# Kernel tuning notes

Measured on AMD Instinct MI355X. Metric: run time of the kernel, lower is better.

The kernel has to match this reference:

```python
import jax, jax.numpy as jnp
import numpy as np

EPS = 1e-5

def _layernorm(x, g, b):
    mu = jnp.mean(x, axis=-1, keepdims=True)
    var = jnp.mean(jnp.square(x - mu), axis=-1, keepdims=True)
    return (x - mu) * jax.lax.rsqrt(var + EPS) * g + b

def _knn_gather(x, idx):
    # x: (B, M, C), idx: (B, N, K) -> (B, N, K, C)
    return jax.vmap(lambda m, i: m[i])(x, idx)

def setup_inputs() -> dict:
    key = jax.random.key(0)
    B, N, M, K, C = 1, 8192, 8192, 32, 256
    ks = jax.random.split(key, 24)
    w = lambda k, *s: (jax.random.normal(k, s, dtype=jnp.float32) * 0.02)
    inp = {
        "input_states": jax.random.normal(ks[0], (B, N, C), dtype=jnp.float32),
        "memory_states": jax.random.normal(ks[1], (B, M, C), dtype=jnp.float32),
        "indices": jax.random.randint(ks[2], (B, N, K), 0, M, dtype=jnp.int32),
        "input_coord": jax.random.normal(ks[3], (B, N, 3), dtype=jnp.float32),
        "memory_coord": jax.random.normal(ks[4], (B, M, 3), dtype=jnp.float32),
        "attention_mask": jnp.ones((B, N, K), dtype=jnp.float32),
        "Wq": w(ks[5], C, C), "bq": jnp.zeros((C,), jnp.float32),
        "Wk": w(ks[6], C, C), "bk": jnp.zeros((C,), jnp.float32),
        "Wv": w(ks[7], C, C), "bv": jnp.zeros((C,), jnp.float32),
        "Wo": w(ks[8], C, C), "bo": jnp.zeros((C,), jnp.float32),
        "ln1_g": jnp.ones((C,), jnp.float32), "ln1_b": jnp.zeros((C,), jnp.float32),
        "Wrpe": w(ks[9], C // 2, 3), "brpe": jnp.zeros((C // 2,), jnp.float32),
        "We": w(ks[10], 2 * C, C), "be": jnp.zeros((2 * C,), jnp.float32),
        "Ws": w(ks[11], C, 2 * C), "bs": jnp.zeros((C,), jnp.float32),
        "ln2_g": jnp.ones((C,), jnp.float32), "ln2_b": jnp.zeros((C,), jnp.float32),
    }
    return inp

def reference(input_states, memory_states, indices, input_coord, memory_coord,
              attention_mask, Wq, bq, Wk, bk, Wv, bv, Wo, bo, ln1_g, ln1_b,
              Wrpe, brpe, We, be, Ws, bs, ln2_g, ln2_b):
    B, N, C = input_states.shape
    H = 8
    Ch = C // H
    q = input_states @ Wq.T + bq                                   # (B,N,C)
    k = _knn_gather(memory_states @ Wk.T + bk, indices)            # (B,N,K,C)
    v = _knn_gather(memory_states @ Wv.T + bv, indices)            # (B,N,K,C)
    # rotary positional encoding on relative coordinates
    rel = _knn_gather(memory_coord, indices) - input_coord[:, :, None, :]  # (B,N,K,3)
    ang = rel @ Wrpe.T + brpe                                      # (B,N,K,C/2)
    cos, sin = jnp.cos(ang), jnp.sin(ang)
    k2 = k.reshape(*k.shape[:-1], C // 2, 2)
    x0, x1 = k2[..., 0], k2[..., 1]
    k = jnp.stack([x0 * cos - x1 * sin, x0 * sin + x1 * cos], axis=-1).reshape(k.shape)
    # multi-head attention over K gathered neighbors
    qh = q.reshape(B, N, H, Ch)
    kh = k.reshape(B, N, -1, H, Ch)
    vh = v.reshape(B, N, -1, H, Ch)
    scores = jnp.einsum('bnhc,bnkhc->bhnk', qh, kh) / np.sqrt(Ch).astype(np.float32)
    scores = scores - 1e6 * (1.0 - attention_mask[:, None, :, :])
    attn = jax.nn.softmax(scores, axis=-1)
    hidden = jnp.einsum('bhnk,bnkhc->bnhc', attn, vh).reshape(B, N, C)
    hidden = hidden @ Wo.T + bo
    out = _layernorm(hidden + input_states, ln1_g, ln1_b)
    ff = jax.nn.relu(out @ We.T + be) @ Ws.T + bs
    return _layernorm(out + ff, ln2_g, ln2_b)
```

## Files before the change

kernel.cpp:

```cpp
#include <hip/hip_runtime.h>
#include <hip/hip_bf16.h>
#include <stdint.h>

typedef __attribute__((ext_vector_type(8))) __bf16 bf16x8;
typedef __attribute__((ext_vector_type(8))) unsigned short u16x8;
typedef __attribute__((ext_vector_type(4))) float f32x4;

__device__ inline float bf2f(unsigned short u) {
  union { unsigned u; float f; } z; z.u = ((unsigned)u) << 16; return z.f;
}
__device__ inline unsigned short f2bf(float f) {
  union { float f; unsigned u; } z; z.f = f;
  unsigned r = z.u + 0x7fffu + ((z.u >> 16) & 1u);
  return (unsigned short)(r >> 16);
}
__device__ inline void gload_lds16(const void* g, void* l) {
  __builtin_amdgcn_global_load_lds((const __attribute__((address_space(1))) void*)g,
                                   (__attribute__((address_space(3))) void*)l, 16, 0, 0);
}

__global__ __launch_bounds__(256, 2) void gemm_proj(
    const float* __restrict__ x, const float* __restrict__ mem,
    const float* __restrict__ Wq, const float* __restrict__ Wk, const float* __restrict__ Wv,
    const float* __restrict__ Wo, const float* __restrict__ We, const float* __restrict__ Ws,
    const float* __restrict__ Wrpe, const float* __restrict__ brpe,
    const float* __restrict__ bq, const float* __restrict__ bk, const float* __restrict__ bv,
    unsigned short* __restrict__ qbuf, unsigned short* __restrict__ kbp,
    unsigned short* __restrict__ vbp,
    unsigned short* __restrict__ wob, unsigned short* __restrict__ web,
    unsigned short* __restrict__ wsb, float4* __restrict__ rpe4) {
  const int tid = threadIdx.x;
  const int by = blockIdx.y;
  const long bm = blockIdx.x;

  if (by == 6) {
#pragma unroll
    for (int it = 0; it < 3; ++it) {
      const int j = (int)bm + 128 * it;
      if (j < 64) {
        const float4 v = *(const float4*)(Wo + (long)j * 1024 + tid * 4);
        ushort4 o; o.x = f2bf(v.x); o.y = f2bf(v.y); o.z = f2bf(v.z); o.w = f2bf(v.w);
        *(ushort4*)(wob + (long)j * 1024 + tid * 4) = o;
      } else if (j < 192) {
        const float4 v = *(const float4*)(We + (long)(j - 64) * 1024 + tid * 4);
        ushort4 o; o.x = f2bf(v.x); o.y = f2bf(v.y); o.z = f2bf(v.z); o.w = f2bf(v.w);
        *(ushort4*)(web + (long)(j - 64) * 1024 + tid * 4) = o;
      } else if (j < 320) {
        const float4 v = *(const float4*)(Ws + (long)(j - 192) * 1024 + tid * 4);
        ushort4 o; o.x = f2bf(v.x); o.y = f2bf(v.y); o.z = f2bf(v.z); o.w = f2bf(v.w);
        *(ushort4*)(wsb + (long)(j - 192) * 1024 + tid * 4) = o;
      } else if (j == 320) {
        if (tid < 128) {
          float4 r;
          r.x = Wrpe[3 * tid]; r.y = Wrpe[3 * tid + 1]; r.z = Wrpe[3 * tid + 2]; r.w = brpe[tid];
          rpe4[tid] = r;
        }
      }
    }
    return;
  }

  __shared__ __attribute__((aligned(16))) char lds[4096 + 8192];
  const int lane = tid & 63;
  const int wm = tid >> 7, wo = (tid >> 6) & 1;

  const float* Ab; const float* Wf; const float* biasp; unsigned short* outp; int cb;
  if (by < 2)      { Ab = x;   Wf = Wq + (long)by * 128 * 256;       biasp = bq + by * 128;       outp = qbuf; cb = by * 128; }
  else if (by < 4) { Ab = mem; Wf = Wk + (long)(by - 2) * 128 * 256; biasp = bk + (by - 2) * 128; outp = kbp;  cb = (by - 2) * 128; }
  else             { Ab = mem; Wf = Wv + (long)(by - 4) * 128 * 256; biasp = bv + (by - 4) * 128; outp = vbp;  cb = (by - 4) * 128; }

  f32x4 acc[2][4] = {};
  for (int kt = 0; kt < 8; ++kt) {
#pragma unroll
    for (int c = 0; c < 2; ++c) {
      const int fb = c * 4096 + tid * 16;
      const int row = fb >> 7, colb = fb & 127;
      const float4 a4 = *(const float4*)((const char*)Ab + (bm * 64 + row) * 1024 + kt * 128 + colb);
      ushort4 o; o.x = f2bf(a4.x); o.y = f2bf(a4.y); o.z = f2bf(a4.z); o.w = f2bf(a4.w);
      *(ushort4*)(lds + row * 64 + (colb >> 1)) = o;
    }
#pragma unroll
    for (int c = 0; c < 4; ++c) {
      const int fb = c * 4096 + tid * 16;
      const int row = fb >> 7, colb = fb & 127;
      const float4 a4 = *(const float4*)((const char*)Wf + (long)row * 1024 + kt * 128 + colb);
      ushort4 o; o.x = f2bf(a4.x); o.y = f2bf(a4.y); o.z = f2bf(a4.z); o.w = f2bf(a4.w);
      *(ushort4*)(lds + 4096 + row * 64 + (colb >> 1)) = o;
    }
    __syncthreads();
    bf16x8 af[2], bfr[4];
    const int kb = (lane >> 4) * 16;
#pragma unroll
    for (int i = 0; i < 2; ++i)
      af[i] = *(const bf16x8*)(lds + (wm * 32 + i * 16 + (lane & 15)) * 64 + kb);
#pragma unroll
    for (int j = 0; j < 4; ++j)
      bfr[j] = *(const bf16x8*)(lds + 4096 + (wo * 64 + j * 16 + (lane & 15)) * 64 + kb);
#pragma unroll
    for (int i = 0; i < 2; ++i)
#pragma unroll
      for (int j = 0; j < 4; ++j)
        acc[i][j] = __builtin_amdgcn_mfma_f32_16x16x32_bf16(af[i], bfr[j], acc[i][j], 0, 0, 0);
    __syncthreads();
  }

#pragma unroll
  for (int i = 0; i < 2; ++i) {
#pragma unroll
    for (int j = 0; j < 4; ++j) {
      const int lc = wo * 64 + j * 16 + (lane & 15);
      const float bvv = biasp[lc];
#pragma unroll
      for (int r = 0; r < 4; ++r) {
        const long rowg = bm * 64 + wm * 32 + i * 16 + (lane >> 4) * 4 + r;
        outp[rowg * 256 + cb + lc] = f2bf(acc[i][j][r] + bvv);
      }
    }
  }
}

__global__ __launch_bounds__(256, 2) void gemm_relu(
    const unsigned short* __restrict__ A,
    const unsigned short* __restrict__ W,
    const float* __restrict__ bias,
    unsigned short* __restrict__ outb) {
  __shared__ __attribute__((aligned(16))) char lds[(64 + 128) * 64];
  const int tid = threadIdx.x, lane = tid & 63;
  const int wm = tid >> 7, wo = (tid >> 6) & 1;
  const long bm = blockIdx.x, bo = blockIdx.y;

  f32x4 acc[2][4] = {};
  const char* Ab = (const char*)(A + bm * 64 * 256);
  const char* Wb = (const char*)(W + bo * 128 * 256);
  for (int kt = 0; kt < 8; ++kt) {
    {
      const int fb = tid * 16;
      gload_lds16(Ab + (long)(fb >> 6) * 512 + kt * 64 + (fb & 63), lds + fb);
    }
#pragma unroll
    for (int c = 0; c < 2; ++c) {
      const int fb = c * 4096 + tid * 16;
      gload_lds16(Wb + (long)(fb >> 6) * 512 + kt * 64 + (fb & 63), lds + 4096 + fb);
    }
    __syncthreads();
    bf16x8 af[2], bfr[4];
    const int kb = (lane >> 4) * 16;
#pragma unroll
    for (int i = 0; i < 2; ++i)
      af[i] = *(const bf16x8*)(lds + (wm * 32 + i * 16 + (lane & 15)) * 64 + kb);
#pragma unroll
    for (int j = 0; j < 4; ++j)
      bfr[j] = *(const bf16x8*)(lds + 4096 + (wo * 64 + j * 16 + (lane & 15)) * 64 + kb);
#pragma unroll
    for (int i = 0; i < 2; ++i)
#pragma unroll
      for (int j = 0; j < 4; ++j)
        acc[i][j] = __builtin_amdgcn_mfma_f32_16x16x32_bf16(af[i], bfr[j], acc[i][j], 0, 0, 0);
    __syncthreads();
  }
#pragma unroll
  for (int i = 0; i < 2; ++i) {
#pragma unroll
    for (int j = 0; j < 4; ++j) {
      const int colg = (int)bo * 128 + wo * 64 + j * 16 + (lane & 15);
      const float bvv = bias[colg];
#pragma unroll
      for (int r = 0; r < 4; ++r) {
        const long rowg = bm * 64 + wm * 32 + i * 16 + (lane >> 4) * 4 + r;
        const float v = acc[i][j][r] + bvv;
        outb[rowg * 512 + colg] = f2bf(v > 0.f ? v : 0.f);
      }
    }
  }
}

template <int KT, int OUT_BF16, int RES_BF16>
__global__ __launch_bounds__(256, 2) void gemm_ln(
    const unsigned short* __restrict__ A,
    const unsigned short* __restrict__ W,
    const float* __restrict__ bias,
    const float* __restrict__ resf,
    const unsigned short* __restrict__ resb,
    const float* __restrict__ g, const float* __restrict__ b,
    float* __restrict__ outf,
    unsigned short* __restrict__ outb) {
  __shared__ __attribute__((aligned(16))) char lds[1024 + 16384];
  __shared__ float2 part[4][16];
  const int tid = threadIdx.x, lane = tid & 63;
  const int wo = tid >> 6;
  const long bm = blockIdx.x;
  constexpr int K = KT * 32;

  f32x4 acc[4] = {};
  const char* Ab = (const char*)(A + bm * 16 * (long)K);
  for (int kt = 0; kt < KT; ++kt) {
    if (tid < 64) {
      const int fb = tid * 16;
      gload_lds16(Ab + (long)(fb >> 6) * (K * 2) + kt * 64 + (fb & 63), lds + fb);
    }
#pragma unroll
    for (int c = 0; c < 4; ++c) {
      const int fb = c * 4096 + tid * 16;
      gload_lds16((const char*)W + (long)(fb >> 6) * (K * 2) + kt * 64 + (fb & 63), lds + 1024 + fb);
    }
    __syncthreads();
    bf16x8 af, bfr[4];
    const int kb = (lane >> 4) * 16;
    af = *(const bf16x8*)(lds + ((lane & 15)) * 64 + kb);
#pragma unroll
    for (int j = 0; j < 4; ++j)
      bfr[j] = *(const bf16x8*)(lds + 1024 + (wo * 64 + j * 16 + (lane & 15)) * 64 + kb);
#pragma unroll
    for (int j = 0; j < 4; ++j)
      acc[j] = __builtin_amdgcn_mfma_f32_16x16x32_bf16(af, bfr[j], acc[j], 0, 0, 0);
    __syncthreads();
  }

  float gj[4], bj[4], biasj[4];
  int colg[4];
#pragma unroll
  for (int j = 0; j < 4; ++j) {
    colg[j] = wo * 64 + j * 16 + (lane & 15);
    gj[j] = g[colg[j]]; bj[j] = b[colg[j]]; biasj[j] = bias[colg[j]];
  }
  float v[4][4];
#pragma unroll
  for (int r = 0; r < 4; ++r) {
    const int row_local = (lane >> 4) * 4 + r;
    const long rowg = bm * 16 + row_local;
    float s = 0.f, s2 = 0.f;
#pragma unroll
    for (int j = 0; j < 4; ++j) {
      const float rv = RES_BF16 ? bf2f(resb[rowg * 256 + colg[j]]) : resf[rowg * 256 + colg[j]];
      float vv = acc[j][r] + biasj[j] + rv;
      v[j][r] = vv;
      s += vv; s2 = fmaf(vv, vv, s2);
    }
#pragma unroll
    for (int m = 8; m > 0; m >>= 1) { s += __shfl_xor(s, m, 16); s2 += __shfl_xor(s2, m, 16); }
    if ((lane & 15) == 0) part[wo][row_local] = make_float2(s, s2);
  }
  __syncthreads();
#pragma unroll
  for (int r = 0; r < 4; ++r) {
    const int row_local = (lane >> 4) * 4 + r;
    const long rowg = bm * 16 + row_local;
    float s = 0.f, s2 = 0.f;
#pragma unroll
    for (int wq = 0; wq < 4; ++wq) { s += part[wq][row_local].x; s2 += part[wq][row_local].y; }
    const float mu = s * (1.f / 256.f);
    const float var = s2 * (1.f / 256.f) - mu * mu;
    const float inv = rsqrtf(var + 1e-5f);
#pragma unroll
    for (int j = 0; j < 4; ++j) {
      const float y = (v[j][r] - mu) * inv * gj[j] + bj[j];
      if (OUT_BF16) outb[rowg * 256 + colg[j]] = f2bf(y);
      else outf[rowg * 256 + colg[j]] = y;
    }
  }
}

__global__ __launch_bounds__(256, 4) void attn2(
    const unsigned short* __restrict__ qb,
    const unsigned short* __restrict__ kbp,
    const unsigned short* __restrict__ vbp,
    const int* __restrict__ idx,
    const float* __restrict__ icoord,
    const float* __restrict__ mcoord,
    const float* __restrict__ mask,
    const float4* __restrict__ rpe4,
    unsigned short* __restrict__ hb)
{
  __shared__ int idx_s[32];
  __shared__ float4 relm_s[32];
  __shared__ float4 rpe_s[128];
  __shared__ float p_s[256];
  __shared__ __attribute__((aligned(16))) unsigned short vls[32][256];

  const int n = blockIdx.x, t = threadIdx.x;
  if (t < 128) rpe_s[t] = rpe4[t];
  if (t < 32) {
    const int m = idx[n * 32 + t];
    idx_s[t] = m;
    float4 rm;
    rm.x = mcoord[(long)m * 3 + 0] - icoord[(long)n * 3 + 0];
    rm.y = mcoord[(long)m * 3 + 1] - icoord[(long)n * 3 + 1];
    rm.z = mcoord[(long)m * 3 + 2] - icoord[(long)n * 3 + 2];
    rm.w = mask[n * 32 + t];
    relm_s[t] = rm;
  }
  __syncthreads();

#pragma unroll
  for (int i = 0; i < 4; ++i) {
    const int b = i * 4096 + t * 16;
    const int r = b >> 9, cb = b & 511;
    gload_lds16((const char*)vbp + (long)idx_s[r] * 512 + cb, (char*)vls + b);
  }

  const int h = t >> 5, k = t & 31;
  const float4 rm = relm_s[k];
  const long krow = idx_s[k];

  u16x8 kv8[4], qv8[4];
  {
    const u16x8* kp = (const u16x8*)(kbp + krow * 256 + h * 32);
    const u16x8* qp = (const u16x8*)(qb + (long)n * 256 + h * 32);
#pragma unroll
    for (int i = 0; i < 4; ++i) { kv8[i] = kp[i]; qv8[i] = qp[i]; }
  }

  float sc = 0.f;
#pragma unroll
  for (int j2 = 0; j2 < 16; ++j2) {
    const float4 wj = rpe_s[h * 16 + j2];
    const float ang = fmaf(wj.x, rm.x, fmaf(wj.y, rm.y, fmaf(wj.z, rm.z, wj.w)));
    float sn, cs;
    __sincosf(ang, &sn, &cs);
    const int wi = j2 >> 2, e0 = (j2 & 3) * 2;
    const float x0 = bf2f(kv8[wi][e0]), x1 = bf2f(kv8[wi][e0 + 1]);
    const float q0 = bf2f(qv8[wi][e0]), q1 = bf2f(qv8[wi][e0 + 1]);
    const float k0 = fmaf(x0, cs, -x1 * sn);
    const float k1 = fmaf(x0, sn, x1 * cs);
    sc = fmaf(q0, k0, sc);
    sc = fmaf(q1, k1, sc);
  }
  sc = sc * 0.17677669529663687f - 1e6f * (1.f - rm.w);

  float mx = sc;
#pragma unroll
  for (int m = 16; m > 0; m >>= 1) mx = fmaxf(mx, __shfl_xor(mx, m, 32));
  const float e = __expf(sc - mx);
  float sum = e;
#pragma unroll
  for (int m = 16; m > 0; m >>= 1) sum += __shfl_xor(sum, m, 32);
  p_s[t] = e / sum;
  __syncthreads();

  float acc = 0.f;
#pragma unroll
  for (int k4 = 0; k4 < 8; ++k4) {
    const float4 p4 = *(const float4*)(p_s + (t >> 5) * 32 + k4 * 4);
    acc = fmaf(p4.x, bf2f(vls[k4 * 4 + 0][t]), acc);
    acc = fmaf(p4.y, bf2f(vls[k4 * 4 + 1][t]), acc);
    acc = fmaf(p4.z, bf2f(vls[k4 * 4 + 2][t]), acc);
    acc = fmaf(p4.w, bf2f(vls[k4 * 4 + 3][t]), acc);
  }
  hb[(long)n * 256 + t] = f2bf(acc);
}

extern "C" void kernel_launch(void* const* d_in, const int* in_sizes, int n_in,
                              void* d_out, int out_size, void* d_ws, size_t ws_size,
                              hipStream_t stream) {
  const float* x    = (const float*)d_in[0];
  const float* mem  = (const float*)d_in[1];
  const int* idx    = (const int*)d_in[2];
  const float* ic   = (const float*)d_in[3];
  const float* mc   = (const float*)d_in[4];
  const float* mask = (const float*)d_in[5];
  const float* Wq = (const float*)d_in[6];  const float* bq = (const float*)d_in[7];
  const float* Wk = (const float*)d_in[8];  const float* bk = (const float*)d_in[9];
  const float* Wv = (const float*)d_in[10]; const float* bv = (const float*)d_in[11];
  const float* Wo = (const float*)d_in[12]; const float* bo = (const float*)d_in[13];
  const float* g1 = (const float*)d_in[14]; const float* b1 = (const float*)d_in[15];
  const float* Wrpe = (const float*)d_in[16]; const float* brpe = (const float*)d_in[17];
  const float* We = (const float*)d_in[18]; const float* be = (const float*)d_in[19];
  const float* Ws = (const float*)d_in[20]; const float* bs = (const float*)d_in[21];
  const float* g2 = (const float*)d_in[22]; const float* b2 = (const float*)d_in[23];

  char* w = (char*)d_ws;
  const size_t MB = 1ull << 20;
  unsigned short* kbp   = (unsigned short*)(w + 0);
  unsigned short* vbp   = (unsigned short*)(w + 4 * MB);
  unsigned short* qbuf  = (unsigned short*)(w + 8 * MB);
  unsigned short* hb    = (unsigned short*)(w + 12 * MB);
  unsigned short* out1b = (unsigned short*)(w + 16 * MB);
  unsigned short* ffb   = (unsigned short*)(w + 20 * MB);
  unsigned short* wob  = (unsigned short*)(w + 28 * MB);
  unsigned short* web  = wob + 65536;
  unsigned short* wsb  = web + 131072;
  float4*         rpe4 = (float4*)(wsb + 131072);

  gemm_proj<<<dim3(128, 7), 256, 0, stream>>>(
      x, mem, Wq, Wk, Wv, Wo, We, Ws, Wrpe, brpe, bq, bk, bv,
      qbuf, kbp, vbp, wob, web, wsb, rpe4);

  attn2<<<8192, 256, 0, stream>>>(qbuf, kbp, vbp, idx, ic, mc, mask, rpe4, hb);

  gemm_ln<8, 1, 0><<<512, 256, 0, stream>>>(
      hb, wob, bo, x, nullptr, g1, b1, nullptr, out1b);

  gemm_relu<<<dim3(128, 4), 256, 0, stream>>>(out1b, web, be, ffb);

  gemm_ln<16, 0, 1><<<512, 256, 0, stream>>>(
      ffb, wsb, bs, nullptr, out1b, g2, b2, (float*)d_out, nullptr);
}
```

Baseline: 82.64 us.

## Interleave K/V per head-half, split attention by half, pre-convert weights

Adds a separate weight-conversion kernel so the QKV projection loads bf16 weights directly into LDS, replacing per-tile fp32 loads and conversions. K and V projections are written into one interleaved buffer laid out per head-half, so each gathered neighbor row is contiguous for one half. Attention is split into 128-thread blocks that each handle half the heads of a point, with a block-index remap that keeps both halves of a point on the same XCD. The intent is better gather locality and occupancy in the dominant attention kernel, at the cost of an extra launch and twice as many blocks.

```diff
diff --git a/kernel.cpp b/kernel.cpp
--- a/kernel.cpp
+++ b/kernel.cpp
@@ -19,55 +19,58 @@
                                    (__attribute__((address_space(3))) void*)l, 16, 0, 0);
 }
 
-__global__ __launch_bounds__(256, 2) void gemm_proj(
-    const float* __restrict__ x, const float* __restrict__ mem,
+__global__ __launch_bounds__(256) void wcvt(
     const float* __restrict__ Wq, const float* __restrict__ Wk, const float* __restrict__ Wv,
     const float* __restrict__ Wo, const float* __restrict__ We, const float* __restrict__ Ws,
     const float* __restrict__ Wrpe, const float* __restrict__ brpe,
-    const float* __restrict__ bq, const float* __restrict__ bk, const float* __restrict__ bv,
-    unsigned short* __restrict__ qbuf, unsigned short* __restrict__ kbp,
-    unsigned short* __restrict__ vbp,
+    unsigned short* __restrict__ wqb, unsigned short* __restrict__ wkvb,
     unsigned short* __restrict__ wob, unsigned short* __restrict__ web,
     unsigned short* __restrict__ wsb, float4* __restrict__ rpe4) {
-  const int tid = threadIdx.x;
+  const int b = blockIdx.x, t = threadIdx.x;
+  const float* src; unsigned short* dst; long off;
+  if (b < 64)       { src = Wq; dst = wqb;           off = (long)b * 1024; }
+  else if (b < 128) { src = Wk; dst = wkvb;          off = (long)(b - 64) * 1024; }
+  else if (b < 192) { src = Wv; dst = wkvb + 65536;  off = (long)(b - 128) * 1024; }
+  else if (b < 256) { src = Wo; dst = wob;           off = (long)(b - 192) * 1024; }
+  else if (b < 384) { src = We; dst = web;           off = (long)(b - 256) * 1024; }
+  else if (b < 512) { src = Ws; dst = wsb;           off = (long)(b - 384) * 1024; }
+  else {
+    if (t < 128) {
+      float4 r;
+      r.x = Wrpe[3 * t]; r.y = Wrpe[3 * t + 1]; r.z = Wrpe[3 * t + 2]; r.w = brpe[t];
+      rpe4[t] = r;
+    }
+    return;
+  }
+  const float4 v = *(const float4*)(src + off + t * 4);
+  ushort4 o;
+  o.x = f2bf(v.x); o.y = f2bf(v.y); o.z = f2bf(v.z); o.w = f2bf(v.w);
+  *(ushort4*)(dst + off + t * 4) = o;
+}
+
+__global__ __launch_bounds__(256, 2) void gemm_proj(
+    const float* __restrict__ x, const float* __restrict__ mem,
+    const unsigned short* __restrict__ wqb, const unsigned short* __restrict__ wkvb,
+    const float* __restrict__ bq, const float* __restrict__ bk, const float* __restrict__ bv,
+    unsigned short* __restrict__ qbuf, unsigned short* __restrict__ kvp) {
+  __shared__ __attribute__((aligned(16))) char lds[4096 + 8192];
+  const int tid = threadIdx.x, lane = tid & 63;
+  const int wm = tid >> 7, wo = (tid >> 6) & 1;
+  const long bm = blockIdx.x;
   const int by = blockIdx.y;
-  const long bm = blockIdx.x;
-
-  if (by == 6) {
-#pragma unroll
-    for (int it = 0; it < 3; ++it) {
-      const int j = (int)bm + 128 * it;
-      if (j < 64) {
-        const float4 v = *(const float4*)(Wo + (long)j * 1024 + tid * 4);
-        ushort4 o; o.x = f2bf(v.x); o.y = f2bf(v.y); o.z = f2bf(v.z); o.w = f2bf(v.w);
-        *(ushort4*)(wob + (long)j * 1024 + tid * 4) = o;
-      } else if (j < 192) {
-        const float4 v = *(const float4*)(We + (long)(j - 64) * 1024 + tid * 4);
-        ushort4 o; o.x = f2bf(v.x); o.y = f2bf(v.y); o.z = f2bf(v.z); o.w = f2bf(v.w);
-        *(ushort4*)(web + (long)(j - 64) * 1024 + tid * 4) = o;
-      } else if (j < 320) {
-        const float4 v = *(const float4*)(Ws + (long)(j - 192) * 1024 + tid * 4);
-        ushort4 o; o.x = f2bf(v.x); o.y = f2bf(v.y); o.z = f2bf(v.z); o.w = f2bf(v.w);
-        *(ushort4*)(wsb + (long)(j - 192) * 1024 + tid * 4) = o;
-      } else if (j == 320) {
-        if (tid < 128) {
-          float4 r;
-          r.x = Wrpe[3 * tid]; r.y = Wrpe[3 * tid + 1]; r.z = Wrpe[3 * tid + 2]; r.w = brpe[tid];
-          rpe4[tid] = r;
-        }
-      }
-    }
-    return;
-  }
-
-  __shared__ __attribute__((aligned(16))) char lds[4096 + 8192];
-  const int lane = tid & 63;
-  const int wm = tid >> 7, wo = (tid >> 6) & 1;
-
-  const float* Ab; const float* Wf; const float* biasp; unsigned short* outp; int cb;
-  if (by < 2)      { Ab = x;   Wf = Wq + (long)by * 128 * 256;       biasp = bq + by * 128;       outp = qbuf; cb = by * 128; }
-  else if (by < 4) { Ab = mem; Wf = Wk + (long)(by - 2) * 128 * 256; biasp = bk + (by - 2) * 128; outp = kbp;  cb = (by - 2) * 128; }
-  else             { Ab = mem; Wf = Wv + (long)(by - 4) * 128 * 256; biasp = bv + (by - 4) * 128; outp = vbp;  cb = (by - 4) * 128; }
+
+  const float* Ab; const unsigned short* Wb; const float* biasp;
+  unsigned short* outp; int obase, ostride;
+  if (by < 2) {
+    Ab = x; Wb = wqb + (long)by * 128 * 256; biasp = bq + by * 128;
+    outp = qbuf; obase = by * 128; ostride = 256;
+  } else if (by < 4) {
+    Ab = mem; Wb = wkvb + (long)(by - 2) * 128 * 256; biasp = bk + (by - 2) * 128;
+    outp = kvp; obase = (by == 2) ? 0 : 256; ostride = 512;
+  } else {
+    Ab = mem; Wb = wkvb + (long)(by - 2) * 128 * 256; biasp = bv + (by - 4) * 128;
+    outp = kvp; obase = (by == 4) ? 128 : 384; ostride = 512;
+  }
 
   f32x4 acc[2][4] = {};
   for (int kt = 0; kt < 8; ++kt) {
@@ -80,12 +83,9 @@
       *(ushort4*)(lds + row * 64 + (colb >> 1)) = o;
     }
 #pragma unroll
-    for (int c = 0; c < 4; ++c) {
+    for (int c = 0; c < 2; ++c) {
       const int fb = c * 4096 + tid * 16;
-      const int row = fb >> 7, colb = fb & 127;
-      const float4 a4 = *(const float4*)((const char*)Wf + (long)row * 1024 + kt * 128 + colb);
-      ushort4 o; o.x = f2bf(a4.x); o.y = f2bf(a4.y); o.z = f2bf(a4.z); o.w = f2bf(a4.w);
-      *(ushort4*)(lds + 4096 + row * 64 + (colb >> 1)) = o;
+      gload_lds16((const char*)Wb + (long)(fb >> 6) * 512 + kt * 64 + (fb & 63), lds + 4096 + fb);
     }
     __syncthreads();
     bf16x8 af[2], bfr[4];
@@ -113,7 +113,7 @@
 #pragma unroll
       for (int r = 0; r < 4; ++r) {
         const long rowg = bm * 64 + wm * 32 + i * 16 + (lane >> 4) * 4 + r;
-        outp[rowg * 256 + cb + lc] = f2bf(acc[i][j][r] + bvv);
+        outp[rowg * ostride + obase + lc] = f2bf(acc[i][j][r] + bvv);
       }
     }
   }
@@ -260,10 +260,9 @@
   }
 }
 
-__global__ __launch_bounds__(256, 4) void attn2(
+__global__ __launch_bounds__(128, 8) void attn3(
     const unsigned short* __restrict__ qb,
-    const unsigned short* __restrict__ kbp,
-    const unsigned short* __restrict__ vbp,
+    const unsigned short* __restrict__ kvp,
     const int* __restrict__ idx,
     const float* __restrict__ icoord,
     const float* __restrict__ mcoord,
@@ -273,12 +272,16 @@
 {
   __shared__ int idx_s[32];
   __shared__ float4 relm_s[32];
-  __shared__ float4 rpe_s[128];
-  __shared__ float p_s[256];
-  __shared__ __attribute__((aligned(16))) unsigned short vls[32][256];
-
-  const int n = blockIdx.x, t = threadIdx.x;
-  if (t < 128) rpe_s[t] = rpe4[t];
+  __shared__ float4 rpe_s[64];
+  __shared__ __attribute__((aligned(16))) float p_s[128];
+  __shared__ __attribute__((aligned(16))) unsigned short vls[32][128];
+
+  const int bid = blockIdx.x, t = threadIdx.x;
+  const int xcd = bid & 7;
+  const int half = xcd >> 2;
+  const int n = (bid >> 3) * 4 + (xcd & 3);
+
+  if (t < 64) rpe_s[t] = rpe4[half * 64 + t];
   if (t < 32) {
     const int m = idx[n * 32 + t];
     idx_s[t] = m;
@@ -293,9 +296,9 @@
 
 #pragma unroll
   for (int i = 0; i < 4; ++i) {
-    const int b = i * 4096 + t * 16;
-    const int r = b >> 9, cb = b & 511;
-    gload_lds16((const char*)vbp + (long)idx_s[r] * 512 + cb, (char*)vls + b);
+    const int b = i * 2048 + t * 16;
+    const int r = b >> 8, cb = b & 255;
+    gload_lds16((const char*)kvp + (long)idx_s[r] * 1024 + half * 512 + 256 + cb, (char*)vls + b);
   }
 
   const int h = t >> 5, k = t & 31;
@@ -304,8 +307,8 @@
 
   u16x8 kv8[4], qv8[4];
   {
-    const u16x8* kp = (const u16x8*)(kbp + krow * 256 + h * 32);
-    const u16x8* qp = (const u16x8*)(qb + (long)n * 256 + h * 32);
+    const u16x8* kp = (const u16x8*)((const char*)kvp + krow * 1024 + half * 512 + h * 64);
+    const u16x8* qp = (const u16x8*)((const char*)qb + (long)n * 512 + half * 256 + h * 64);
 #pragma unroll
     for (int i = 0; i < 4; ++i) { kv8[i] = kp[i]; qv8[i] = qp[i]; }
   }
@@ -338,15 +341,16 @@
   __syncthreads();
 
   float acc = 0.f;
+  const int h2 = t >> 5;
 #pragma unroll
   for (int k4 = 0; k4 < 8; ++k4) {
-    const float4 p4 = *(const float4*)(p_s + (t >> 5) * 32 + k4 * 4);
+    const float4 p4 = *(const float4*)(p_s + h2 * 32 + k4 * 4);
     acc = fmaf(p4.x, bf2f(vls[k4 * 4 + 0][t]), acc);
     acc = fmaf(p4.y, bf2f(vls[k4 * 4 + 1][t]), acc);
     acc = fmaf(p4.z, bf2f(vls[k4 * 4 + 2][t]), acc);
     acc = fmaf(p4.w, bf2f(vls[k4 * 4 + 3][t]), acc);
   }
-  hb[(long)n * 256 + t] = f2bf(acc);
+  hb[(long)n * 256 + half * 128 + t] = f2bf(acc);
 }
 
 extern "C" void kernel_launch(void* const* d_in, const int* in_sizes, int n_in,
@@ -370,22 +374,24 @@
 
   char* w = (char*)d_ws;
   const size_t MB = 1ull << 20;
-  unsigned short* kbp   = (unsigned short*)(w + 0);
-  unsigned short* vbp   = (unsigned short*)(w + 4 * MB);
+  unsigned short* kvp   = (unsigned short*)(w + 0);
   unsigned short* qbuf  = (unsigned short*)(w + 8 * MB);
   unsigned short* hb    = (unsigned short*)(w + 12 * MB);
   unsigned short* out1b = (unsigned short*)(w + 16 * MB);
   unsigned short* ffb   = (unsigned short*)(w + 20 * MB);
-  unsigned short* wob  = (unsigned short*)(w + 28 * MB);
+  unsigned short* wqb  = (unsigned short*)(w + 28 * MB);
+  unsigned short* wkvb = wqb + 65536;
+  unsigned short* wob  = wkvb + 131072;
   unsigned short* web  = wob + 65536;
   unsigned short* wsb  = web + 131072;
   float4*         rpe4 = (float4*)(wsb + 131072);
 
-  gemm_proj<<<dim3(128, 7), 256, 0, stream>>>(
-      x, mem, Wq, Wk, Wv, Wo, We, Ws, Wrpe, brpe, bq, bk, bv,
-      qbuf, kbp, vbp, wob, web, wsb, rpe4);
-
-  attn2<<<8192, 256, 0, stream>>>(qbuf, kbp, vbp, idx, ic, mc, mask, rpe4, hb);
+  wcvt<<<513, 256, 0, stream>>>(Wq, Wk, Wv, Wo, We, Ws, Wrpe, brpe,
+                                wqb, wkvb, wob, web, wsb, rpe4);
+
+  gemm_proj<<<dim3(128, 6), 256, 0, stream>>>(x, mem, wqb, wkvb, bq, bk, bv, qbuf, kvp);
+
+  attn3<<<16384, 128, 0, stream>>>(qbuf, kvp, idx, ic, mc, mask, rpe4, hb);
 
   gemm_ln<8, 1, 0><<<512, 256, 0, stream>>>(
       hb, wob, bo, x, nullptr, g1, b1, nullptr, out1b);
```

After: 83.99 us. Within noise of the previous version (+1.6%).

## Fuse output projection, LN1, FFN expand/relu/squeeze and LN2 into one kernel

Applied to the files above, without the earlier changes.

Replaces the three tail kernels (Wo GEMM + LayerNorm, relu expand GEMM, squeeze GEMM + LayerNorm) with a single megatail kernel. Each block handles 32 rows and keeps the intermediate out1 and FFN activations in 64KB of LDS, so they no longer round-trip through global memory and two launches disappear. The cost is a grid of only 256 blocks with 64KB LDS each, which means low occupancy, no double buffering of weight tiles, and all weights being re-streamed by every block.

```diff
diff --git a/kernel.cpp b/kernel.cpp
--- a/kernel.cpp
+++ b/kernel.cpp
@@ -119,147 +119,6 @@
   }
 }
 
-__global__ __launch_bounds__(256, 2) void gemm_relu(
-    const unsigned short* __restrict__ A,
-    const unsigned short* __restrict__ W,
-    const float* __restrict__ bias,
-    unsigned short* __restrict__ outb) {
-  __shared__ __attribute__((aligned(16))) char lds[(64 + 128) * 64];
-  const int tid = threadIdx.x, lane = tid & 63;
-  const int wm = tid >> 7, wo = (tid >> 6) & 1;
-  const long bm = blockIdx.x, bo = blockIdx.y;
-
-  f32x4 acc[2][4] = {};
-  const char* Ab = (const char*)(A + bm * 64 * 256);
-  const char* Wb = (const char*)(W + bo * 128 * 256);
-  for (int kt = 0; kt < 8; ++kt) {
-    {
-      const int fb = tid * 16;
-      gload_lds16(Ab + (long)(fb >> 6) * 512 + kt * 64 + (fb & 63), lds + fb);
-    }
-#pragma unroll
-    for (int c = 0; c < 2; ++c) {
-      const int fb = c * 4096 + tid * 16;
-      gload_lds16(Wb + (long)(fb >> 6) * 512 + kt * 64 + (fb & 63), lds + 4096 + fb);
-    }
-    __syncthreads();
-    bf16x8 af[2], bfr[4];
-    const int kb = (lane >> 4) * 16;
-#pragma unroll
-    for (int i = 0; i < 2; ++i)
-      af[i] = *(const bf16x8*)(lds + (wm * 32 + i * 16 + (lane & 15)) * 64 + kb);
-#pragma unroll
-    for (int j = 0; j < 4; ++j)
-      bfr[j] = *(const bf16x8*)(lds + 4096 + (wo * 64 + j * 16 + (lane & 15)) * 64 + kb);
-#pragma unroll
-    for (int i = 0; i < 2; ++i)
-#pragma unroll
-      for (int j = 0; j < 4; ++j)
-        acc[i][j] = __builtin_amdgcn_mfma_f32_16x16x32_bf16(af[i], bfr[j], acc[i][j], 0, 0, 0);
-    __syncthreads();
-  }
-#pragma unroll
-  for (int i = 0; i < 2; ++i) {
-#pragma unroll
-    for (int j = 0; j < 4; ++j) {
-      const int colg = (int)bo * 128 + wo * 64 + j * 16 + (lane & 15);
-      const float bvv = bias[colg];
-#pragma unroll
-      for (int r = 0; r < 4; ++r) {
-        const long rowg = bm * 64 + wm * 32 + i * 16 + (lane >> 4) * 4 + r;
-        const float v = acc[i][j][r] + bvv;
-        outb[rowg * 512 + colg] = f2bf(v > 0.f ? v : 0.f);
-      }
-    }
-  }
-}
-
-template <int KT, int OUT_BF16, int RES_BF16>
-__global__ __launch_bounds__(256, 2) void gemm_ln(
-    const unsigned short* __restrict__ A,
-    const unsigned short* __restrict__ W,
-    const float* __restrict__ bias,
-    const float* __restrict__ resf,
-    const unsigned short* __restrict__ resb,
-    const float* __restrict__ g, const float* __restrict__ b,
-    float* __restrict__ outf,
-    unsigned short* __restrict__ outb) {
-  __shared__ __attribute__((aligned(16))) char lds[1024 + 16384];
-  __shared__ float2 part[4][16];
-  const int tid = threadIdx.x, lane = tid & 63;
-  const int wo = tid >> 6;
-  const long bm = blockIdx.x;
-  constexpr int K = KT * 32;
-
-  f32x4 acc[4] = {};
-  const char* Ab = (const char*)(A + bm * 16 * (long)K);
-  for (int kt = 0; kt < KT; ++kt) {
-    if (tid < 64) {
-      const int fb = tid * 16;
-      gload_lds16(Ab + (long)(fb >> 6) * (K * 2) + kt * 64 + (fb & 63), lds + fb);
-    }
-#pragma unroll
-    for (int c = 0; c < 4; ++c) {
-      const int fb = c * 4096 + tid * 16;
-      gload_lds16((const char*)W + (long)(fb >> 6) * (K * 2) + kt * 64 + (fb & 63), lds + 1024 + fb);
-    }
-    __syncthreads();
-    bf16x8 af, bfr[4];
-    const int kb = (lane >> 4) * 16;
-    af = *(const bf16x8*)(lds + ((lane & 15)) * 64 + kb);
-#pragma unroll
-    for (int j = 0; j < 4; ++j)
-      bfr[j] = *(const bf16x8*)(lds + 1024 + (wo * 64 + j * 16 + (lane & 15)) * 64 + kb);
-#pragma unroll
-    for (int j = 0; j < 4; ++j)
-      acc[j] = __builtin_amdgcn_mfma_f32_16x16x32_bf16(af, bfr[j], acc[j], 0, 0, 0);
-    __syncthreads();
-  }
-
-  float gj[4], bj[4], biasj[4];
-  int colg[4];
-#pragma unroll
-  for (int j = 0; j < 4; ++j) {
-    colg[j] = wo * 64 + j * 16 + (lane & 15);
-    gj[j] = g[colg[j]]; bj[j] = b[colg[j]]; biasj[j] = bias[colg[j]];
-  }
-  float v[4][4];
-#pragma unroll
-  for (int r = 0; r < 4; ++r) {
-    const int row_local = (lane >> 4) * 4 + r;
-    const long rowg = bm * 16 + row_local;
-    float s = 0.f, s2 = 0.f;
-#pragma unroll
-    for (int j = 0; j < 4; ++j) {
-      const float rv = RES_BF16 ? bf2f(resb[rowg * 256 + colg[j]]) : resf[rowg * 256 + colg[j]];
-      float vv = acc[j][r] + biasj[j] + rv;
-      v[j][r] = vv;
-      s += vv; s2 = fmaf(vv, vv, s2);
-    }
-#pragma unroll
-    for (int m = 8; m > 0; m >>= 1) { s += __shfl_xor(s, m, 16); s2 += __shfl_xor(s2, m, 16); }
-    if ((lane & 15) == 0) part[wo][row_local] = make_float2(s, s2);
-  }
-  __syncthreads();
-#pragma unroll
-  for (int r = 0; r < 4; ++r) {
-    const int row_local = (lane >> 4) * 4 + r;
-    const long rowg = bm * 16 + row_local;
-    float s = 0.f, s2 = 0.f;
-#pragma unroll
-    for (int wq = 0; wq < 4; ++wq) { s += part[wq][row_local].x; s2 += part[wq][row_local].y; }
-    const float mu = s * (1.f / 256.f);
-    const float var = s2 * (1.f / 256.f) - mu * mu;
-    const float inv = rsqrtf(var + 1e-5f);
-#pragma unroll
-    for (int j = 0; j < 4; ++j) {
-      const float y = (v[j][r] - mu) * inv * gj[j] + bj[j];
-      if (OUT_BF16) outb[rowg * 256 + colg[j]] = f2bf(y);
-      else outf[rowg * 256 + colg[j]] = y;
-    }
-  }
-}
-
 __global__ __launch_bounds__(256, 4) void attn2(
     const unsigned short* __restrict__ qb,
     const unsigned short* __restrict__ kbp,
@@ -347,6 +206,211 @@
     acc = fmaf(p4.w, bf2f(vls[k4 * 4 + 3][t]), acc);
   }
   hb[(long)n * 256 + t] = f2bf(acc);
+}
+
+__global__ __launch_bounds__(256) void megatail(
+    const unsigned short* __restrict__ hb, const float* __restrict__ x,
+    const unsigned short* __restrict__ wob, const unsigned short* __restrict__ web,
+    const unsigned short* __restrict__ wsb,
+    const float* __restrict__ bo, const float* __restrict__ g1, const float* __restrict__ b1,
+    const float* __restrict__ be, const float* __restrict__ bs,
+    const float* __restrict__ g2, const float* __restrict__ b2,
+    float* __restrict__ outf) {
+  __shared__ __attribute__((aligned(16))) char lds[65536];
+  char* const out1_l = lds;
+  char* const ffa_l  = lds + 16384;
+  char* const wt_l   = lds + 49152;
+  float2* const part = (float2*)(lds + 49152);
+
+  const int tid = threadIdx.x, lane = tid & 63;
+  const int wv = tid >> 6;
+  const long bm = blockIdx.x;
+  const int kb = (lane >> 4) * 16;
+  const int lrow = (lane >> 4) * 4;
+  const int c15 = lane & 15;
+  int colg[4];
+#pragma unroll
+  for (int j = 0; j < 4; ++j) colg[j] = wv * 64 + j * 16 + c15;
+
+  f32x4 acc[2][4];
+
+#pragma unroll
+  for (int p = 0; p < 4; ++p) {
+    const int b = p * 4096 + tid * 16;
+    gload_lds16((const char*)hb + (bm * 32 + (b >> 9)) * 512 + (b & 511), ffa_l + b);
+  }
+#pragma unroll
+  for (int i = 0; i < 2; ++i)
+#pragma unroll
+    for (int j = 0; j < 4; ++j) acc[i][j] = (f32x4){0.f, 0.f, 0.f, 0.f};
+
+  for (int kt = 0; kt < 8; ++kt) {
+#pragma unroll
+    for (int c = 0; c < 4; ++c) {
+      const int b = c * 4096 + tid * 16;
+      gload_lds16((const char*)wob + (long)(b >> 6) * 512 + kt * 64 + (b & 63), wt_l + b);
+    }
+    __syncthreads();
+    bf16x8 af[2], bfq[4];
+#pragma unroll
+    for (int i = 0; i < 2; ++i)
+      af[i] = *(const bf16x8*)(ffa_l + (i * 16 + c15) * 512 + kt * 64 + kb);
+#pragma unroll
+    for (int j = 0; j < 4; ++j)
+      bfq[j] = *(const bf16x8*)(wt_l + (wv * 64 + j * 16 + c15) * 64 + kb);
+#pragma unroll
+    for (int i = 0; i < 2; ++i)
+#pragma unroll
+      for (int j = 0; j < 4; ++j)
+        acc[i][j] = __builtin_amdgcn_mfma_f32_16x16x32_bf16(af[i], bfq[j], acc[i][j], 0, 0, 0);
+    __syncthreads();
+  }
+
+#pragma unroll
+  for (int i = 0; i < 2; ++i)
+#pragma unroll
+    for (int r = 0; r < 4; ++r) {
+      const int rl = i * 16 + lrow + r;
+      const long rowg = bm * 32 + rl;
+#pragma unroll
+      for (int j = 0; j < 4; ++j)
+        acc[i][j][r] += bo[colg[j]] + x[rowg * 256 + colg[j]];
+    }
+#pragma unroll
+  for (int i = 0; i < 2; ++i)
+#pragma unroll
+    for (int r = 0; r < 4; ++r) {
+      const int rl = i * 16 + lrow + r;
+      float s = 0.f, s2 = 0.f;
+#pragma unroll
+      for (int j = 0; j < 4; ++j) { const float v = acc[i][j][r]; s += v; s2 = fmaf(v, v, s2); }
+#pragma unroll
+      for (int m = 8; m > 0; m >>= 1) { s += __shfl_xor(s, m, 16); s2 += __shfl_xor(s2, m, 16); }
+      if (c15 == 0) part[wv * 32 + rl] = make_float2(s, s2);
+    }
+  __syncthreads();
+#pragma unroll
+  for (int i = 0; i < 2; ++i)
+#pragma unroll
+    for (int r = 0; r < 4; ++r) {
+      const int rl = i * 16 + lrow + r;
+      float s = 0.f, s2 = 0.f;
+#pragma unroll
+      for (int q = 0; q < 4; ++q) { s += part[q * 32 + rl].x; s2 += part[q * 32 + rl].y; }
+      const float mu = s * (1.f / 256.f);
+      const float var = s2 * (1.f / 256.f) - mu * mu;
+      const float inv = rsqrtf(var + 1e-5f);
+#pragma unroll
+      for (int j = 0; j < 4; ++j) {
+        const float y = (acc[i][j][r] - mu) * inv * g1[colg[j]] + b1[colg[j]];
+        *(unsigned short*)(out1_l + rl * 512 + colg[j] * 2) = f2bf(y);
+      }
+    }
+  __syncthreads();
+
+  for (int hc = 0; hc < 2; ++hc) {
+#pragma unroll
+    for (int i = 0; i < 2; ++i)
+#pragma unroll
+      for (int j = 0; j < 4; ++j) acc[i][j] = (f32x4){0.f, 0.f, 0.f, 0.f};
+    for (int kt = 0; kt < 8; ++kt) {
+#pragma unroll
+      for (int c = 0; c < 4; ++c) {
+        const int b = c * 4096 + tid * 16;
+        gload_lds16((const char*)web + ((long)hc * 256 + (b >> 6)) * 512 + kt * 64 + (b & 63), wt_l + b);
+      }
+      __syncthreads();
+      bf16x8 af[2], bfq[4];
+#pragma unroll
+      for (int i = 0; i < 2; ++i)
+        af[i] = *(const bf16x8*)(out1_l + (i * 16 + c15) * 512 + kt * 64 + kb);
+#pragma unroll
+      for (int j = 0; j < 4; ++j)
+        bfq[j] = *(const bf16x8*)(wt_l + (wv * 64 + j * 16 + c15) * 64 + kb);
+#pragma unroll
+      for (int i = 0; i < 2; ++i)
+#pragma unroll
+        for (int j = 0; j < 4; ++j)
+          acc[i][j] = __builtin_amdgcn_mfma_f32_16x16x32_bf16(af[i], bfq[j], acc[i][j], 0, 0, 0);
+      __syncthreads();
+    }
+#pragma unroll
+    for (int i = 0; i < 2; ++i)
+#pragma unroll
+      for (int r = 0; r < 4; ++r) {
+        const int rl = i * 16 + lrow + r;
+#pragma unroll
+        for (int j = 0; j < 4; ++j) {
+          const int col = hc * 256 + colg[j];
+          const float v = acc[i][j][r] + be[col];
+          *(unsigned short*)(ffa_l + rl * 1024 + col * 2) = f2bf(v > 0.f ? v : 0.f);
+        }
+      }
+  }
+
+#pragma unroll
+  for (int i = 0; i < 2; ++i)
+#pragma unroll
+    for (int j = 0; j < 4; ++j) acc[i][j] = (f32x4){0.f, 0.f, 0.f, 0.f};
+  for (int kt = 0; kt < 16; ++kt) {
+#pragma unroll
+    for (int c = 0; c < 4; ++c) {
+      const int b = c * 4096 + tid * 16;
+      gload_lds16((const char*)wsb + (long)(b >> 6) * 1024 + kt * 64 + (b & 63), wt_l + b);
+    }
+    __syncthreads();
+    bf16x8 af[2], bfq[4];
+#pragma unroll
+    for (int i = 0; i < 2; ++i)
+      af[i] = *(const bf16x8*)(ffa_l + (i * 16 + c15) * 1024 + kt * 64 + kb);
+#pragma unroll
+    for (int j = 0; j < 4; ++j)
+      bfq[j] = *(const bf16x8*)(wt_l + (wv * 64 + j * 16 + c15) * 64 + kb);
+#pragma unroll
+    for (int i = 0; i < 2; ++i)
+#pragma unroll
+      for (int j = 0; j < 4; ++j)
+        acc[i][j] = __builtin_amdgcn_mfma_f32_16x16x32_bf16(af[i], bfq[j], acc[i][j], 0, 0, 0);
+    __syncthreads();
+  }
+#pragma unroll
+  for (int i = 0; i < 2; ++i)
+#pragma unroll
+    for (int r = 0; r < 4; ++r) {
+      const int rl = i * 16 + lrow + r;
+#pragma unroll
+      for (int j = 0; j < 4; ++j)
+        acc[i][j][r] += bs[colg[j]] + bf2f(*(const unsigned short*)(out1_l + rl * 512 + colg[j] * 2));
+    }
+#pragma unroll
+  for (int i = 0; i < 2; ++i)
+#pragma unroll
+    for (int r = 0; r < 4; ++r) {
+      const int rl = i * 16 + lrow + r;
+      float s = 0.f, s2 = 0.f;
+#pragma unroll
+      for (int j = 0; j < 4; ++j) { const float v = acc[i][j][r]; s += v; s2 = fmaf(v, v, s2); }
+#pragma unroll
+      for (int m = 8; m > 0; m >>= 1) { s += __shfl_xor(s, m, 16); s2 += __shfl_xor(s2, m, 16); }
+      if (c15 == 0) part[wv * 32 + rl] = make_float2(s, s2);
+    }
+  __syncthreads();
+#pragma unroll
+  for (int i = 0; i < 2; ++i)
+#pragma unroll
+    for (int r = 0; r < 4; ++r) {
+      const int rl = i * 16 + lrow + r;
+      const long rowg = bm * 32 + rl;
+      float s = 0.f, s2 = 0.f;
+#pragma unroll
+      for (int q = 0; q < 4; ++q) { s += part[q * 32 + rl].x; s2 += part[q * 32 + rl].y; }
+      const float mu = s * (1.f / 256.f);
+      const float var = s2 * (1.f / 256.f) - mu * mu;
+      const float inv = rsqrtf(var + 1e-5f);
+#pragma unroll
+      for (int j = 0; j < 4; ++j)
+        outf[rowg * 256 + colg[j]] = (acc[i][j][r] - mu) * inv * g2[colg[j]] + b2[colg[j]];
+    }
 }
 
 extern "C" void kernel_launch(void* const* d_in, const int* in_sizes, int n_in,
@@ -370,13 +434,11 @@
 
   char* w = (char*)d_ws;
   const size_t MB = 1ull << 20;
-  unsigned short* kbp   = (unsigned short*)(w + 0);
-  unsigned short* vbp   = (unsigned short*)(w + 4 * MB);
-  unsigned short* qbuf  = (unsigned short*)(w + 8 * MB);
-  unsigned short* hb    = (unsigned short*)(w + 12 * MB);
-  unsigned short* out1b = (unsigned short*)(w + 16 * MB);
-  unsigned short* ffb   = (unsigned short*)(w + 20 * MB);
-  unsigned short* wob  = (unsigned short*)(w + 28 * MB);
+  unsigned short* kbp  = (unsigned short*)(w + 0);
+  unsigned short* vbp  = (unsigned short*)(w + 4 * MB);
+  unsigned short* qbuf = (unsigned short*)(w + 8 * MB);
+  unsigned short* hb   = (unsigned short*)(w + 12 * MB);
+  unsigned short* wob  = (unsigned short*)(w + 16 * MB);
   unsigned short* web  = wob + 65536;
   unsigned short* wsb  = web + 131072;
   float4*         rpe4 = (float4*)(wsb + 131072);
@@ -387,11 +449,6 @@
 
   attn2<<<8192, 256, 0, stream>>>(qbuf, kbp, vbp, idx, ic, mc, mask, rpe4, hb);
 
-  gemm_ln<8, 1, 0><<<512, 256, 0, stream>>>(
-      hb, wob, bo, x, nullptr, g1, b1, nullptr, out1b);
-
-  gemm_relu<<<dim3(128, 4), 256, 0, stream>>>(out1b, web, be, ffb);
-
-  gemm_ln<16, 0, 1><<<512, 256, 0, stream>>>(
-      ffb, wsb, bs, nullptr, out1b, g2, b2, (float*)d_out, nullptr);
-}
+  megatail<<<256, 256, 0, stream>>>(hb, x, wob, web, wsb,
+                                    bo, g1, b1, be, bs, g2, b2, (float*)d_out);
+}
```

Measured after the change: 84.72 us. 1.03x slower.
